# Optimization experiments

Hardware: AMD Instinct MI355X
Metric: run time of the kernel (lower is better)

Reference implementation:

```python
import jax, jax.numpy as jnp
import numpy as np

E = 65536          # number of edges (cell pairs)
D = 256            # hidden_dim
P = 8              # n_lr_pairs


def setup_inputs() -> dict:
    key = jax.random.key(0)
    k1, k2, k3, k4, k5, k6, k7 = jax.random.split(key, 7)
    scale = 1.0 / np.sqrt(D)
    z_src = jax.random.normal(k1, (E, D), dtype=jnp.float32)
    z_dst = jax.random.normal(k2, (E, D), dtype=jnp.float32)
    lr_pair_idx = jax.random.randint(k3, (E,), 0, P, dtype=jnp.int64)
    # Per-LR-pair Linear(D, D): y = x @ W.T + b  (torch convention, W: [out, in])
    W_lr = jax.random.normal(k4, (P, D, D), dtype=jnp.float32) * scale
    b_lr = jax.random.normal(k5, (P, D), dtype=jnp.float32) * scale
    # nn.Bilinear(D, D, 1): weight [1, D, D], bias [1]
    W_bil = jax.random.normal(k6, (1, D, D), dtype=jnp.float32) * scale
    b_bil = jax.random.normal(k7, (1,), dtype=jnp.float32) * scale
    return {"z_src": z_src, "z_dst": z_dst, "W_lr": W_lr, "b_lr": b_lr,
            "W_bil": W_bil, "b_bil": b_bil, "lr_pair_idx": lr_pair_idx}


def _forward(z_src, z_dst, W_lr, b_lr, W_bil, b_bil, lr_pair_idx):
    # Per-LR-pair linear projection of z_src (MoE-style routing).
    # Fixed small loop over P experts; each iteration is a dense GEMM over
    # all E edges, masked to the edges routed to that pair. All idx values
    # lie in [0, P), so the zeros-init in the original is fully overwritten.
    z_proj = jnp.zeros_like(z_src)
    for p in range(P):
        mask = (lr_pair_idx == p)[:, None]                      # [E, 1]
        y_p = z_src @ W_lr[p].T + b_lr[p]                       # [E, D]
        z_proj = jnp.where(mask, y_p, z_proj)
    # Bilinear scoring: score_e = z_proj_e @ W_bil[0] @ z_dst_e + b_bil
    t = z_proj @ W_bil[0]                                       # [E, D]
    scores = jnp.sum(t * z_dst, axis=-1, keepdims=True) + b_bil  # [E, 1]
    return scores


def reference(z_src, z_dst, W_lr, b_lr, W_bil, b_bil, lr_pair_idx):
    return _forward(z_src, z_dst, W_lr, b_lr, W_bil, b_bil, lr_pair_idx)
```

## Files before the change

### kernel.cpp

```cpp
#include <hip/hip_runtime.h>
#include <hip/hip_bf16.h>
#include <cstddef>

#define NE 65536
#define ND 256
#define NP 8
#define RBLK 64
#define EPB (NE / RBLK)

typedef short bf16x8 __attribute__((ext_vector_type(8)));
typedef float f32x4  __attribute__((ext_vector_type(4)));

__device__ __forceinline__ unsigned short f2bf(float f) {
  unsigned int u = __float_as_uint(f);
  u += 0x7FFFu + ((u >> 16) & 1u);
  return (unsigned short)(u >> 16);
}

__device__ __forceinline__ int sniff_is32(const void* idxraw, int* lflag) {
  int tid = threadIdx.x;
  if (tid == 0) *lflag = 0;
  __syncthreads();
  const unsigned int* w = (const unsigned int*)idxraw;
  unsigned int val = w[(blockIdx.x * 256 + tid) * 2 + 1];
  if (__any(val != 0) && (tid & 63) == 0) atomicOr(lflag, 1);
  __syncthreads();
  return *lflag;
}

__device__ __forceinline__ int load_idx(const void* idxraw, int is32, int e) {
  return is32 ? ((const int*)idxraw)[e] : (int)((const long long*)idxraw)[e];
}

__global__ __launch_bounds__(256) void k_hist(const void* __restrict__ idxraw,
                                              int* __restrict__ counts) {
  __shared__ int h[NP];
  __shared__ int lflag;
  int tid = threadIdx.x;
  int is32 = sniff_is32(idxraw, &lflag);
  if (tid < NP) h[tid] = 0;
  __syncthreads();
  int base = blockIdx.x * EPB;
#pragma unroll
  for (int i = 0; i < EPB / 256; ++i) {
    int p = load_idx(idxraw, is32, base + tid + i * 256);
    atomicAdd(&h[p], 1);
  }
  __syncthreads();
  if (tid < NP) counts[blockIdx.x * NP + tid] = h[tid];
}

__global__ __launch_bounds__(64) void k_scan(const int* __restrict__ counts,
                                             int* __restrict__ hdr,
                                             int* __restrict__ bases) {
  __shared__ int cnt[NP];
  __shared__ int off[NP + 1];
  int q = threadIdx.x;
  if (q < NP) {
    int s = 0;
    for (int b = 0; b < RBLK; ++b) s += counts[b * NP + q];
    cnt[q] = s;
  }
  __syncthreads();
  if (q == 0) {
    int o = 0, tt = 0;
    for (int p = 0; p < NP; ++p) {
      off[p] = o;
      hdr[p] = o;
      hdr[9 + p] = tt;
      o += cnt[p];
      tt += (cnt[p] + 63) >> 6;
    }
    off[NP] = o;
    hdr[NP] = o;
    hdr[9 + NP] = tt;
  }
  __syncthreads();
  if (q < NP) {
    int run = off[q];
    for (int b = 0; b < RBLK; ++b) {
      bases[b * NP + q] = run;
      run += counts[b * NP + q];
    }
  }
}

__global__ __launch_bounds__(256) void k_scatter(const void* __restrict__ idxraw,
                                                 const int* __restrict__ bases,
                                                 int* __restrict__ perm) {
  __shared__ int cur[NP];
  __shared__ int lflag;
  int tid = threadIdx.x;
  int is32 = sniff_is32(idxraw, &lflag);
  if (tid < NP) cur[tid] = bases[blockIdx.x * NP + tid];
  __syncthreads();
  int base = blockIdx.x * EPB;
#pragma unroll
  for (int i = 0; i < EPB / 256; ++i) {
    int e = base + tid + i * 256;
    int p = load_idx(idxraw, is32, e);
    int slot = atomicAdd(&cur[p], 1);
    perm[slot] = e;
  }
}

__global__ __launch_bounds__(256) void k_prep(const float* __restrict__ Wbil,
                                              const float* __restrict__ blr,
                                              unsigned short* __restrict__ WbT,
                                              float* __restrict__ v) {
  int b = blockIdx.x, t = threadIdx.x;
  if (b < 32) {
    int s = b * 256 + t;
    int kt = s >> 10, c = (s >> 6) & 15, l = s & 63;
    int col = c * 16 + (l & 15);
    int k0 = kt * 32 + (l >> 4) * 8;
    union { uint4 u; unsigned short h[8]; } uu;
#pragma unroll
    for (int j = 0; j < 8; ++j)
      uu.h[j] = f2bf(Wbil[(k0 + j) * ND + col]);
    *(uint4*)(WbT + (size_t)s * 8) = uu.u;
  } else {
    int p = b - 32;
    float s = 0.f;
    for (int k = 0; k < ND; ++k)
      s = fmaf(blr[p * ND + k], Wbil[k * ND + t], s);
    v[p * ND + t] = s;
  }
}

__global__ __launch_bounds__(256) void k_cpre(const float* __restrict__ Wlr,
                                              const unsigned short* __restrict__ WbT,
                                              unsigned short* __restrict__ Cst) {
  __shared__ unsigned short aF[2048 * 8];
  int blk = blockIdx.x;
  int p = blk >> 2;
  int i0 = (blk & 3) * 64;
  int tid = threadIdx.x;
  const float* Wp = Wlr + (size_t)p * ND * ND;
#pragma unroll
  for (int it = 0; it < 8; ++it) {
    int s = tid + it * 256;
    int kt = s >> 8, r = (s >> 6) & 3, l = s & 63;
    int i = r * 16 + (l & 15);
    int k0 = kt * 32 + (l >> 4) * 8;
    union { uint4 u; unsigned short h[8]; } uu;
#pragma unroll
    for (int j = 0; j < 8; ++j)
      uu.h[j] = f2bf(Wp[(size_t)(k0 + j) * ND + i0 + i]);
    *(uint4*)(aF + (size_t)s * 8) = uu.u;
  }
  __syncthreads();
  int w = tid >> 6, l = tid & 63;
  f32x4 zero = {0.f, 0.f, 0.f, 0.f};
  f32x4 acc[16];
#pragma unroll
  for (int c = 0; c < 16; ++c) acc[c] = zero;
  for (int kt = 0; kt < 8; ++kt) {
    bf16x8 a = *(const bf16x8*)(aF + (size_t)((kt * 4 + w) * 64 + l) * 8);
#pragma unroll
    for (int c = 0; c < 16; ++c) {
      bf16x8 bb = *(const bf16x8*)(WbT + (size_t)((kt * 16 + c) * 64 + l) * 8);
      acc[c] = __builtin_amdgcn_mfma_f32_16x16x32_bf16(a, bb, acc[c], 0, 0, 0);
    }
  }
  unsigned short* Cp = Cst + (size_t)p * ND * ND;
#pragma unroll
  for (int c = 0; c < 16; ++c) {
#pragma unroll
    for (int q = 0; q < 4; ++q) {
      int i = i0 + w * 16 + ((l >> 4) * 4) + q;
      int j = c * 16 + (l & 15);
      int pos = ((i >> 5) * 16 + (j >> 4)) * 512 + (((i >> 3) & 3) * 16 + (j & 15)) * 8 + (i & 7);
      Cp[pos] = f2bf(acc[c][q]);
    }
  }
}

__global__ __launch_bounds__(256, 2) void k_main(const float* __restrict__ zsrc,
                                                 const float* __restrict__ zdst,
                                                 const int* __restrict__ perm,
                                                 const int* __restrict__ hdr,
                                                 const unsigned short* __restrict__ Cst,
                                                 const float* __restrict__ v,
                                                 const float* __restrict__ bbil,
                                                 float* __restrict__ out) {
  __shared__ unsigned short aF[2048 * 8];
  __shared__ unsigned short zL[64 * 256];
  __shared__ int eids[64];
  __shared__ int shdr[18];
  __shared__ float red[4][64];
  int tid = threadIdx.x;
  if (tid < 18) shdr[tid] = hdr[tid];
  __syncthreads();
  int bid = blockIdx.x;
  if (bid >= shdr[9 + NP]) return;
  int p = 0;
  while (p < NP - 1 && bid >= shdr[9 + p + 1]) ++p;
  int t = bid - shdr[9 + p];
  int cnt = shdr[p + 1] - shdr[p];
  int ebase = shdr[p] + t * 64;
  int nrow = cnt - t * 64; if (nrow > 64) nrow = 64;
  if (tid < 64) {
    int r = tid < nrow ? tid : nrow - 1;
    eids[tid] = perm[ebase + r];
  }
  __syncthreads();
  int w = tid >> 6, l = tid & 63;
#pragma unroll
  for (int i = 0; i < 16; ++i) {
    int row = w * 16 + i;
    int e = eids[row];
    f32x4 fs = ((const f32x4*)(zsrc + (size_t)e * ND))[l];
    f32x4 fd = ((const f32x4*)(zdst + (size_t)e * ND))[l];
    union { ushort4 u; unsigned short h[4]; } us, ud;
#pragma unroll
    for (int j = 0; j < 4; ++j) { us.h[j] = f2bf(fs[j]); ud.h[j] = f2bf(fd[j]); }
    *(ushort4*)((char*)zL + row * 512 + l * 8) = ud.u;
    int slot = ((l >> 3) * 4 + w) * 64 + ((l & 7) >> 1) * 16 + i;
    *(ushort4*)((char*)aF + slot * 16 + (l & 1) * 8) = us.u;
  }
  __syncthreads();

  const unsigned short* Cp = Cst + (size_t)p * ND * ND;
  f32x4 zero = {0.f, 0.f, 0.f, 0.f};
  f32x4 acc[4][4];
#pragma unroll
  for (int r = 0; r < 4; ++r)
#pragma unroll
    for (int c = 0; c < 4; ++c) acc[r][c] = zero;
#pragma unroll
  for (int kt = 0; kt < 8; ++kt) {
    bf16x8 a[4];
#pragma unroll
    for (int r = 0; r < 4; ++r)
      a[r] = *(const bf16x8*)(aF + (size_t)((kt * 4 + r) * 64 + l) * 8);
#pragma unroll
    for (int cl = 0; cl < 4; ++cl) {
      bf16x8 bb = *(const bf16x8*)(Cp + (size_t)((kt * 16 + w * 4 + cl) * 64 + l) * 8);
#pragma unroll
      for (int r = 0; r < 4; ++r)
        acc[r][cl] = __builtin_amdgcn_mfma_f32_16x16x32_bf16(a[r], bb, acc[r][cl], 0, 0, 0);
    }
  }
  float vloc[4];
#pragma unroll
  for (int cl = 0; cl < 4; ++cl)
    vloc[cl] = v[p * ND + (w * 4 + cl) * 16 + (l & 15)];
#pragma unroll
  for (int r = 0; r < 4; ++r) {
#pragma unroll
    for (int q = 0; q < 4; ++q) {
      int row = r * 16 + ((l >> 4) * 4) + q;
      float sv = 0.f;
#pragma unroll
      for (int cl = 0; cl < 4; ++cl) {
        int col = (w * 4 + cl) * 16 + (l & 15);
        unsigned short hz = zL[row * 256 + col];
        float zv = __uint_as_float(((unsigned int)hz) << 16);
        sv = fmaf(acc[r][cl][q] + vloc[cl], zv, sv);
      }
      sv += __shfl_xor(sv, 1, 64);
      sv += __shfl_xor(sv, 2, 64);
      sv += __shfl_xor(sv, 4, 64);
      sv += __shfl_xor(sv, 8, 64);
      if ((l & 15) == 0) red[w][row] = sv;
    }
  }
  __syncthreads();
  if (tid < 64 && tid < nrow) {
    float sc = red[0][tid] + red[1][tid] + red[2][tid] + red[3][tid] + bbil[0];
    out[eids[tid]] = sc;
  }
}

extern "C" void kernel_launch(void* const* d_in, const int* in_sizes, int n_in,
                              void* d_out, int out_size, void* d_ws, size_t ws_size,
                              hipStream_t stream) {
  const float* zsrc = (const float*)d_in[0];
  const float* zdst = (const float*)d_in[1];
  const float* Wlr  = (const float*)d_in[2];
  const float* blr  = (const float*)d_in[3];
  const float* Wbil = (const float*)d_in[4];
  const float* bbil = (const float*)d_in[5];
  const void*  idx  = (const void*)d_in[6];
  float* out = (float*)d_out;

  char* ws = (char*)d_ws;
  int* hdr    = (int*)ws;
  int* counts = (int*)(ws + 4096);
  int* bases  = (int*)(ws + 8192);
  int* perm   = (int*)(ws + 16384);
  unsigned short* WbT = (unsigned short*)(ws + 16384 + (size_t)NE * 4);
  float* v = (float*)(ws + 16384 + (size_t)NE * 4 + 131072);
  unsigned short* Cst = (unsigned short*)(ws + 16384 + (size_t)NE * 4 + 131072 + 8192);

  k_prep<<<40, 256, 0, stream>>>(Wbil, blr, WbT, v);
  k_hist<<<RBLK, 256, 0, stream>>>(idx, counts);
  k_scan<<<1, 64, 0, stream>>>(counts, hdr, bases);
  k_scatter<<<RBLK, 256, 0, stream>>>(idx, bases, perm);
  k_cpre<<<32, 256, 0, stream>>>(Wlr, WbT, Cst);
  k_main<<<1032, 256, 0, stream>>>(zsrc, zdst, perm, hdr, Cst, v, bbil, out);
}
```

Baseline: 88.96 us.

## Pre-permute bf16 activations into tile-packed buffers during scatter, contiguous loads in main

Adds a scatter kernel that, besides building the permutation, gathers z_src and z_dst rows, converts them to bf16, and writes them into per-tile packed buffers already laid out as MFMA fragments and swizzled LDS rows. The main kernel then streams each 32KB tile contiguously into LDS instead of gathering fp32 rows per edge. The histogram and scatter grids grow to 256 blocks, and the zdst LDS layout gets an XOR swizzle to reduce bank conflicts. The cost is an extra write and read of packed bf16 activations through global memory, plus an extra kernel stage. A fallback path keeps the old gather when the workspace is too small.

```diff
diff --git a/kernel.cpp b/kernel.cpp
--- a/kernel.cpp
+++ b/kernel.cpp
@@ -1,12 +1,14 @@
 #include <hip/hip_runtime.h>
 #include <hip/hip_bf16.h>
 #include <cstddef>
+#include <cstdint>
 
 #define NE 65536
 #define ND 256
 #define NP 8
-#define RBLK 64
+#define RBLK 256
 #define EPB (NE / RBLK)
+#define MAXT 1032
 
 typedef short bf16x8 __attribute__((ext_vector_type(8)));
 typedef float f32x4  __attribute__((ext_vector_type(4)));
@@ -22,7 +24,7 @@
   if (tid == 0) *lflag = 0;
   __syncthreads();
   const unsigned int* w = (const unsigned int*)idxraw;
-  unsigned int val = w[(blockIdx.x * 256 + tid) * 2 + 1];
+  unsigned int val = w[((blockIdx.x & 63) * 256 + tid) * 2 + 1];
   if (__any(val != 0) && (tid & 63) == 0) atomicOr(lflag, 1);
   __syncthreads();
   return *lflag;
@@ -40,12 +42,8 @@
   int is32 = sniff_is32(idxraw, &lflag);
   if (tid < NP) h[tid] = 0;
   __syncthreads();
-  int base = blockIdx.x * EPB;
-#pragma unroll
-  for (int i = 0; i < EPB / 256; ++i) {
-    int p = load_idx(idxraw, is32, base + tid + i * 256);
-    atomicAdd(&h[p], 1);
-  }
+  int p = load_idx(idxraw, is32, blockIdx.x * EPB + tid);
+  atomicAdd(&h[p], 1);
   __syncthreads();
   if (tid < NP) counts[blockIdx.x * NP + tid] = h[tid];
 }
@@ -65,15 +63,11 @@
   if (q == 0) {
     int o = 0, tt = 0;
     for (int p = 0; p < NP; ++p) {
-      off[p] = o;
-      hdr[p] = o;
-      hdr[9 + p] = tt;
+      off[p] = o; hdr[p] = o; hdr[9 + p] = tt;
       o += cnt[p];
       tt += (cnt[p] + 63) >> 6;
     }
-    off[NP] = o;
-    hdr[NP] = o;
-    hdr[9 + NP] = tt;
+    off[NP] = o; hdr[NP] = o; hdr[9 + NP] = tt;
   }
   __syncthreads();
   if (q < NP) {
@@ -85,6 +79,50 @@
   }
 }
 
+__global__ __launch_bounds__(256) void k_scatter_mv(const void* __restrict__ idxraw,
+                                                    const float* __restrict__ zsrc,
+                                                    const float* __restrict__ zdst,
+                                                    const int* __restrict__ hdr,
+                                                    const int* __restrict__ bases,
+                                                    int* __restrict__ perm,
+                                                    unsigned short* __restrict__ zsrcP,
+                                                    unsigned short* __restrict__ zdstP) {
+  __shared__ int cur[NP];
+  __shared__ int soff[NP], stb[NP];
+  __shared__ int lflag;
+  int tid = threadIdx.x;
+  int is32 = sniff_is32(idxraw, &lflag);
+  if (tid < NP) {
+    cur[tid] = bases[blockIdx.x * NP + tid];
+    soff[tid] = hdr[tid];
+    stb[tid] = hdr[9 + tid];
+  }
+  __syncthreads();
+  int w = tid >> 6, l = tid & 63;
+  int e = blockIdx.x * EPB + w * 64 + l;
+  int p = load_idx(idxraw, is32, e);
+  int slot = atomicAdd(&cur[p], 1);
+  perm[slot] = e;
+  int local = slot - soff[p];
+  int tile = stb[p] + (local >> 6);
+  int row = local & 63;
+  int c0 = l * 4;
+#pragma unroll 8
+  for (int i = 0; i < 64; ++i) {
+    int ei = __shfl(e, i, 64);
+    int ti = __shfl(tile, i, 64);
+    int ri = __shfl(row, i, 64);
+    float4 fs = *(const float4*)(zsrc + (size_t)ei * ND + c0);
+    float4 fd = *(const float4*)(zdst + (size_t)ei * ND + c0);
+    union { unsigned long long u; unsigned short h[4]; } us, ud;
+    us.h[0] = f2bf(fs.x); us.h[1] = f2bf(fs.y); us.h[2] = f2bf(fs.z); us.h[3] = f2bf(fs.w);
+    ud.h[0] = f2bf(fd.x); ud.h[1] = f2bf(fd.y); ud.h[2] = f2bf(fd.z); ud.h[3] = f2bf(fd.w);
+    int fslot = ((c0 >> 5) * 4 + (ri >> 4)) * 64 + ((c0 & 31) >> 3) * 16 + (ri & 15);
+    *(unsigned long long*)((char*)zsrcP + (size_t)ti * 32768 + fslot * 16 + (c0 & 7) * 2) = us.u;
+    *(unsigned long long*)((char*)zdstP + (size_t)ti * 32768 + ri * 512 + ((l * 8) ^ ((ri & 7) << 4))) = ud.u;
+  }
+}
+
 __global__ __launch_bounds__(256) void k_scatter(const void* __restrict__ idxraw,
                                                  const int* __restrict__ bases,
                                                  int* __restrict__ perm) {
@@ -94,14 +132,10 @@
   int is32 = sniff_is32(idxraw, &lflag);
   if (tid < NP) cur[tid] = bases[blockIdx.x * NP + tid];
   __syncthreads();
-  int base = blockIdx.x * EPB;
-#pragma unroll
-  for (int i = 0; i < EPB / 256; ++i) {
-    int e = base + tid + i * 256;
-    int p = load_idx(idxraw, is32, e);
-    int slot = atomicAdd(&cur[p], 1);
-    perm[slot] = e;
-  }
+  int e = blockIdx.x * EPB + tid;
+  int p = load_idx(idxraw, is32, e);
+  int slot = atomicAdd(&cur[p], 1);
+  perm[slot] = e;
 }
 
 __global__ __launch_bounds__(256) void k_prep(const float* __restrict__ Wbil,
@@ -176,14 +210,14 @@
   }
 }
 
-__global__ __launch_bounds__(256, 2) void k_main(const float* __restrict__ zsrc,
-                                                 const float* __restrict__ zdst,
-                                                 const int* __restrict__ perm,
-                                                 const int* __restrict__ hdr,
-                                                 const unsigned short* __restrict__ Cst,
-                                                 const float* __restrict__ v,
-                                                 const float* __restrict__ bbil,
-                                                 float* __restrict__ out) {
+__global__ __launch_bounds__(256, 2) void k_main_f(const unsigned short* __restrict__ zsrcP,
+                                                   const unsigned short* __restrict__ zdstP,
+                                                   const int* __restrict__ perm,
+                                                   const int* __restrict__ hdr,
+                                                   const unsigned short* __restrict__ Cst,
+                                                   const float* __restrict__ v,
+                                                   const float* __restrict__ bbil,
+                                                   float* __restrict__ out) {
   __shared__ unsigned short aF[2048 * 8];
   __shared__ unsigned short zL[64 * 256];
   __shared__ int eids[64];
@@ -200,10 +234,100 @@
   int cnt = shdr[p + 1] - shdr[p];
   int ebase = shdr[p] + t * 64;
   int nrow = cnt - t * 64; if (nrow > 64) nrow = 64;
-  if (tid < 64) {
-    int r = tid < nrow ? tid : nrow - 1;
-    eids[tid] = perm[ebase + r];
-  }
+  if (tid < 64) eids[tid] = perm[ebase + (tid < nrow ? tid : nrow - 1)];
+  const uint4* gA = (const uint4*)((const char*)zsrcP + (size_t)bid * 32768);
+  const uint4* gZ = (const uint4*)((const char*)zdstP + (size_t)bid * 32768);
+  uint4 ra[8], rz[8];
+#pragma unroll
+  for (int i = 0; i < 8; ++i) ra[i] = gA[i * 256 + tid];
+#pragma unroll
+  for (int i = 0; i < 8; ++i) rz[i] = gZ[i * 256 + tid];
+#pragma unroll
+  for (int i = 0; i < 8; ++i) ((uint4*)aF)[i * 256 + tid] = ra[i];
+#pragma unroll
+  for (int i = 0; i < 8; ++i) ((uint4*)zL)[i * 256 + tid] = rz[i];
+  __syncthreads();
+
+  int w = tid >> 6, l = tid & 63;
+  const unsigned short* Cp = Cst + (size_t)p * ND * ND;
+  f32x4 zero = {0.f, 0.f, 0.f, 0.f};
+  f32x4 acc[4][4];
+#pragma unroll
+  for (int r = 0; r < 4; ++r)
+#pragma unroll
+    for (int c = 0; c < 4; ++c) acc[r][c] = zero;
+#pragma unroll
+  for (int kt = 0; kt < 8; ++kt) {
+    bf16x8 a[4];
+#pragma unroll
+    for (int r = 0; r < 4; ++r)
+      a[r] = *(const bf16x8*)(aF + (size_t)((kt * 4 + r) * 64 + l) * 8);
+#pragma unroll
+    for (int cl = 0; cl < 4; ++cl) {
+      bf16x8 bb = *(const bf16x8*)(Cp + (size_t)((kt * 16 + w * 4 + cl) * 64 + l) * 8);
+#pragma unroll
+      for (int r = 0; r < 4; ++r)
+        acc[r][cl] = __builtin_amdgcn_mfma_f32_16x16x32_bf16(a[r], bb, acc[r][cl], 0, 0, 0);
+    }
+  }
+  float vloc[4];
+#pragma unroll
+  for (int cl = 0; cl < 4; ++cl)
+    vloc[cl] = v[p * ND + (w * 4 + cl) * 16 + (l & 15)];
+#pragma unroll
+  for (int r = 0; r < 4; ++r) {
+#pragma unroll
+    for (int q = 0; q < 4; ++q) {
+      int row = r * 16 + ((l >> 4) * 4) + q;
+      unsigned int swz = (unsigned int)((row & 7) << 4);
+      float sv = 0.f;
+#pragma unroll
+      for (int cl = 0; cl < 4; ++cl) {
+        int col = (w * 4 + cl) * 16 + (l & 15);
+        unsigned int zb = (unsigned int)(row * 512) + (((unsigned int)(col * 2)) ^ swz);
+        unsigned short hz = *(const unsigned short*)((const char*)zL + zb);
+        float zv = __uint_as_float(((unsigned int)hz) << 16);
+        sv = fmaf(acc[r][cl][q] + vloc[cl], zv, sv);
+      }
+      sv += __shfl_xor(sv, 1, 64);
+      sv += __shfl_xor(sv, 2, 64);
+      sv += __shfl_xor(sv, 4, 64);
+      sv += __shfl_xor(sv, 8, 64);
+      if ((l & 15) == 0) red[w][row] = sv;
+    }
+  }
+  __syncthreads();
+  if (tid < 64 && tid < nrow) {
+    float sc = red[0][tid] + red[1][tid] + red[2][tid] + red[3][tid] + bbil[0];
+    out[eids[tid]] = sc;
+  }
+}
+
+__global__ __launch_bounds__(256, 2) void k_main_g(const float* __restrict__ zsrc,
+                                                   const float* __restrict__ zdst,
+                                                   const int* __restrict__ perm,
+                                                   const int* __restrict__ hdr,
+                                                   const unsigned short* __restrict__ Cst,
+                                                   const float* __restrict__ v,
+                                                   const float* __restrict__ bbil,
+                                                   float* __restrict__ out) {
+  __shared__ unsigned short aF[2048 * 8];
+  __shared__ unsigned short zL[64 * 256];
+  __shared__ int eids[64];
+  __shared__ int shdr[18];
+  __shared__ float red[4][64];
+  int tid = threadIdx.x;
+  if (tid < 18) shdr[tid] = hdr[tid];
+  __syncthreads();
+  int bid = blockIdx.x;
+  if (bid >= shdr[9 + NP]) return;
+  int p = 0;
+  while (p < NP - 1 && bid >= shdr[9 + p + 1]) ++p;
+  int t = bid - shdr[9 + p];
+  int cnt = shdr[p + 1] - shdr[p];
+  int ebase = shdr[p] + t * 64;
+  int nrow = cnt - t * 64; if (nrow > 64) nrow = 64;
+  if (tid < 64) eids[tid] = perm[ebase + (tid < nrow ? tid : nrow - 1)];
   __syncthreads();
   int w = tid >> 6, l = tid & 63;
 #pragma unroll
@@ -215,12 +339,11 @@
     union { ushort4 u; unsigned short h[4]; } us, ud;
 #pragma unroll
     for (int j = 0; j < 4; ++j) { us.h[j] = f2bf(fs[j]); ud.h[j] = f2bf(fd[j]); }
-    *(ushort4*)((char*)zL + row * 512 + l * 8) = ud.u;
+    *(ushort4*)((char*)zL + row * 512 + ((l * 8) ^ ((row & 7) << 4))) = ud.u;
     int slot = ((l >> 3) * 4 + w) * 64 + ((l & 7) >> 1) * 16 + i;
     *(ushort4*)((char*)aF + slot * 16 + (l & 1) * 8) = us.u;
   }
   __syncthreads();
-
   const unsigned short* Cp = Cst + (size_t)p * ND * ND;
   f32x4 zero = {0.f, 0.f, 0.f, 0.f};
   f32x4 acc[4][4];
@@ -251,11 +374,13 @@
 #pragma unroll
     for (int q = 0; q < 4; ++q) {
       int row = r * 16 + ((l >> 4) * 4) + q;
+      unsigned int swz = (unsigned int)((row & 7) << 4);
       float sv = 0.f;
 #pragma unroll
       for (int cl = 0; cl < 4; ++cl) {
         int col = (w * 4 + cl) * 16 + (l & 15);
-        unsigned short hz = zL[row * 256 + col];
+        unsigned int zb = (unsigned int)(row * 512) + (((unsigned int)(col * 2)) ^ swz);
+        unsigned short hz = *(const unsigned short*)((const char*)zL + zb);
         float zv = __uint_as_float(((unsigned int)hz) << 16);
         sv = fmaf(acc[r][cl][q] + vloc[cl], zv, sv);
       }
@@ -288,16 +413,25 @@
   char* ws = (char*)d_ws;
   int* hdr    = (int*)ws;
   int* counts = (int*)(ws + 4096);
-  int* bases  = (int*)(ws + 8192);
-  int* perm   = (int*)(ws + 16384);
-  unsigned short* WbT = (unsigned short*)(ws + 16384 + (size_t)NE * 4);
-  float* v = (float*)(ws + 16384 + (size_t)NE * 4 + 131072);
-  unsigned short* Cst = (unsigned short*)(ws + 16384 + (size_t)NE * 4 + 131072 + 8192);
+  int* bases  = (int*)(ws + 12288);
+  int* perm   = (int*)(ws + 20480);
+  unsigned short* WbT = (unsigned short*)(ws + 282624);
+  float* v            = (float*)(ws + 413696);
+  unsigned short* Cst = (unsigned short*)(ws + 421888);
+  size_t zoff = 2097152;
+  unsigned short* zsrcP = (unsigned short*)(ws + zoff);
+  unsigned short* zdstP = (unsigned short*)(ws + zoff + (size_t)MAXT * 32768);
+  size_t need = zoff + 2ull * (size_t)MAXT * 32768;
 
   k_prep<<<40, 256, 0, stream>>>(Wbil, blr, WbT, v);
   k_hist<<<RBLK, 256, 0, stream>>>(idx, counts);
   k_scan<<<1, 64, 0, stream>>>(counts, hdr, bases);
-  k_scatter<<<RBLK, 256, 0, stream>>>(idx, bases, perm);
   k_cpre<<<32, 256, 0, stream>>>(Wlr, WbT, Cst);
-  k_main<<<1032, 256, 0, stream>>>(zsrc, zdst, perm, hdr, Cst, v, bbil, out);
-}
+  if (ws_size >= need) {
+    k_scatter_mv<<<RBLK, 256, 0, stream>>>(idx, zsrc, zdst, hdr, bases, perm, zsrcP, zdstP);
+    k_main_f<<<MAXT, 256, 0, stream>>>(zsrcP, zdstP, perm, hdr, Cst, v, bbil, out);
+  } else {
+    k_scatter<<<RBLK, 256, 0, stream>>>(idx, bases, perm);
+    k_main_g<<<MAXT, 256, 0, stream>>>(zsrc, zdst, perm, hdr, Cst, v, bbil, out);
+  }
+}
```

New measurement: 128.9 us. +44.9%, slower.

## Use 512-thread blocks in main kernel with XOR-swizzled LDS layouts

Applied to the files above, without the earlier changes.

The main fused kernel goes from 256 to 512 threads per block, so each of 8 waves handles half as many output column tiles and the accumulator register footprint halves. Launch bounds now ask for 4 blocks per CU. LDS writes and reads for the staged z_src fragments and z_dst rows get XOR swizzles to cut bank conflicts, and the final reduction sums 8 partial buffers. The risk is more B-operand (Cst) loads per block and higher LDS use per CU, which may cap how many blocks actually fit.

```diff
diff --git a/kernel.cpp b/kernel.cpp
--- a/kernel.cpp
+++ b/kernel.cpp
@@ -7,6 +7,7 @@
 #define NP 8
 #define RBLK 64
 #define EPB (NE / RBLK)
+#define MAXT 1032
 
 typedef short bf16x8 __attribute__((ext_vector_type(8)));
 typedef float f32x4  __attribute__((ext_vector_type(4)));
@@ -16,18 +17,20 @@
   u += 0x7FFFu + ((u >> 16) & 1u);
   return (unsigned short)(u >> 16);
 }
+__device__ __forceinline__ float bf2f(unsigned short h) {
+  return __uint_as_float(((unsigned int)h) << 16);
+}
 
 __device__ __forceinline__ int sniff_is32(const void* idxraw, int* lflag) {
   int tid = threadIdx.x;
   if (tid == 0) *lflag = 0;
   __syncthreads();
   const unsigned int* w = (const unsigned int*)idxraw;
-  unsigned int val = w[(blockIdx.x * 256 + tid) * 2 + 1];
+  unsigned int val = w[((blockIdx.x & 63) * 256 + (tid & 255)) * 2 + 1];
   if (__any(val != 0) && (tid & 63) == 0) atomicOr(lflag, 1);
   __syncthreads();
   return *lflag;
 }
-
 __device__ __forceinline__ int load_idx(const void* idxraw, int is32, int e) {
   return is32 ? ((const int*)idxraw)[e] : (int)((const long long*)idxraw)[e];
 }
@@ -65,15 +68,11 @@
   if (q == 0) {
     int o = 0, tt = 0;
     for (int p = 0; p < NP; ++p) {
-      off[p] = o;
-      hdr[p] = o;
-      hdr[9 + p] = tt;
+      off[p] = o; hdr[p] = o; hdr[9 + p] = tt;
       o += cnt[p];
       tt += (cnt[p] + 63) >> 6;
     }
-    off[NP] = o;
-    hdr[NP] = o;
-    hdr[9 + NP] = tt;
+    off[NP] = o; hdr[NP] = o; hdr[9 + NP] = tt;
   }
   __syncthreads();
   if (q < NP) {
@@ -176,7 +175,7 @@
   }
 }
 
-__global__ __launch_bounds__(256, 2) void k_main(const float* __restrict__ zsrc,
+__global__ __launch_bounds__(512, 4) void k_main(const float* __restrict__ zsrc,
                                                  const float* __restrict__ zdst,
                                                  const int* __restrict__ perm,
                                                  const int* __restrict__ hdr,
@@ -184,11 +183,11 @@
                                                  const float* __restrict__ v,
                                                  const float* __restrict__ bbil,
                                                  float* __restrict__ out) {
-  __shared__ unsigned short aF[2048 * 8];
-  __shared__ unsigned short zL[64 * 256];
+  __shared__ unsigned short aF[16384];
+  __shared__ unsigned short zL[16384];
+  __shared__ float red[8][64];
   __shared__ int eids[64];
   __shared__ int shdr[18];
-  __shared__ float red[4][64];
   int tid = threadIdx.x;
   if (tid < 18) shdr[tid] = hdr[tid];
   __syncthreads();
@@ -200,64 +199,69 @@
   int cnt = shdr[p + 1] - shdr[p];
   int ebase = shdr[p] + t * 64;
   int nrow = cnt - t * 64; if (nrow > 64) nrow = 64;
-  if (tid < 64) {
-    int r = tid < nrow ? tid : nrow - 1;
-    eids[tid] = perm[ebase + r];
-  }
+  if (tid < 64) eids[tid] = perm[ebase + (tid < nrow ? tid : nrow - 1)];
   __syncthreads();
   int w = tid >> 6, l = tid & 63;
-#pragma unroll
-  for (int i = 0; i < 16; ++i) {
-    int row = w * 16 + i;
+
+  int kt0 = l >> 3, pos0 = (l & 7) >> 1, par0 = l & 1;
+#pragma unroll
+  for (int i = 0; i < 8; ++i) {
+    int row = w * 8 + i;
     int e = eids[row];
-    f32x4 fs = ((const f32x4*)(zsrc + (size_t)e * ND))[l];
-    f32x4 fd = ((const f32x4*)(zdst + (size_t)e * ND))[l];
-    union { ushort4 u; unsigned short h[4]; } us, ud;
-#pragma unroll
-    for (int j = 0; j < 4; ++j) { us.h[j] = f2bf(fs[j]); ud.h[j] = f2bf(fd[j]); }
-    *(ushort4*)((char*)zL + row * 512 + l * 8) = ud.u;
-    int slot = ((l >> 3) * 4 + w) * 64 + ((l & 7) >> 1) * 16 + i;
-    *(ushort4*)((char*)aF + slot * 16 + (l & 1) * 8) = us.u;
+    float4 fs = *(const float4*)(zsrc + (size_t)e * ND + l * 4);
+    float4 fd = *(const float4*)(zdst + (size_t)e * ND + l * 4);
+    union { ushort4 u; unsigned short hh[4]; } us, ud;
+    us.hh[0] = f2bf(fs.x); us.hh[1] = f2bf(fs.y); us.hh[2] = f2bf(fs.z); us.hh[3] = f2bf(fs.w);
+    ud.hh[0] = f2bf(fd.x); ud.hh[1] = f2bf(fd.y); ud.hh[2] = f2bf(fd.z); ud.hh[3] = f2bf(fd.w);
+    *(ushort4*)((char*)zL + row * 512 + ((l * 8) ^ ((row & 7) << 4))) = ud.u;
+    unsigned byte = (unsigned)(((kt0 * 4 + (row >> 4)) << 10) | (pos0 << 8) | ((row & 15) << 4) | (par0 << 3));
+    byte ^= (unsigned)(((kt0 & 3) << 5) ^ ((pos0 & 1) << 4));
+    *(ushort4*)((char*)aF + byte) = us.u;
   }
   __syncthreads();
 
   const unsigned short* Cp = Cst + (size_t)p * ND * ND;
   f32x4 zero = {0.f, 0.f, 0.f, 0.f};
-  f32x4 acc[4][4];
-#pragma unroll
-  for (int r = 0; r < 4; ++r)
-#pragma unroll
-    for (int c = 0; c < 4; ++c) acc[r][c] = zero;
+  f32x4 acc[4][2];
+#pragma unroll
+  for (int sr = 0; sr < 4; ++sr)
+#pragma unroll
+    for (int cl = 0; cl < 2; ++cl) acc[sr][cl] = zero;
+  int pos = l >> 4;
 #pragma unroll
   for (int kt = 0; kt < 8; ++kt) {
     bf16x8 a[4];
 #pragma unroll
-    for (int r = 0; r < 4; ++r)
-      a[r] = *(const bf16x8*)(aF + (size_t)((kt * 4 + r) * 64 + l) * 8);
-#pragma unroll
-    for (int cl = 0; cl < 4; ++cl) {
-      bf16x8 bb = *(const bf16x8*)(Cp + (size_t)((kt * 16 + w * 4 + cl) * 64 + l) * 8);
-#pragma unroll
-      for (int r = 0; r < 4; ++r)
-        acc[r][cl] = __builtin_amdgcn_mfma_f32_16x16x32_bf16(a[r], bb, acc[r][cl], 0, 0, 0);
-    }
-  }
-  float vloc[4];
-#pragma unroll
-  for (int cl = 0; cl < 4; ++cl)
-    vloc[cl] = v[p * ND + (w * 4 + cl) * 16 + (l & 15)];
-#pragma unroll
-  for (int r = 0; r < 4; ++r) {
+    for (int sr = 0; sr < 4; ++sr) {
+      unsigned byte = (unsigned)(((kt * 4 + sr) << 10) | (pos << 8) | ((l & 15) << 4));
+      byte ^= (unsigned)(((kt & 3) << 5) ^ ((pos & 1) << 4));
+      a[sr] = *(const bf16x8*)((const char*)aF + byte);
+    }
+#pragma unroll
+    for (int cl = 0; cl < 2; ++cl) {
+      bf16x8 bb = *(const bf16x8*)(Cp + (size_t)((kt * 16 + (w * 2 + cl)) * 64 + l) * 8);
+#pragma unroll
+      for (int sr = 0; sr < 4; ++sr)
+        acc[sr][cl] = __builtin_amdgcn_mfma_f32_16x16x32_bf16(a[sr], bb, acc[sr][cl], 0, 0, 0);
+    }
+  }
+
+  float vloc[2];
+#pragma unroll
+  for (int cl = 0; cl < 2; ++cl)
+    vloc[cl] = v[p * ND + (w * 2 + cl) * 16 + (l & 15)];
+#pragma unroll
+  for (int sr = 0; sr < 4; ++sr) {
 #pragma unroll
     for (int q = 0; q < 4; ++q) {
-      int row = r * 16 + ((l >> 4) * 4) + q;
+      int row = sr * 16 + (l >> 4) * 4 + q;
+      unsigned swz = (unsigned)((row & 7) << 4);
       float sv = 0.f;
 #pragma unroll
-      for (int cl = 0; cl < 4; ++cl) {
-        int col = (w * 4 + cl) * 16 + (l & 15);
-        unsigned short hz = zL[row * 256 + col];
-        float zv = __uint_as_float(((unsigned int)hz) << 16);
-        sv = fmaf(acc[r][cl][q] + vloc[cl], zv, sv);
+      for (int cl = 0; cl < 2; ++cl) {
+        int col = (w * 2 + cl) * 16 + (l & 15);
+        unsigned zb = (unsigned)(row * 512) + (((unsigned)(col * 2)) ^ swz);
+        sv = fmaf(acc[sr][cl][q] + vloc[cl], bf2f(*(const unsigned short*)((const char*)zL + zb)), sv);
       }
       sv += __shfl_xor(sv, 1, 64);
       sv += __shfl_xor(sv, 2, 64);
@@ -268,7 +272,9 @@
   }
   __syncthreads();
   if (tid < 64 && tid < nrow) {
-    float sc = red[0][tid] + red[1][tid] + red[2][tid] + red[3][tid] + bbil[0];
+    float sc = bbil[0];
+#pragma unroll
+    for (int ww = 0; ww < 8; ++ww) sc += red[ww][tid];
     out[eids[tid]] = sc;
   }
 }
@@ -299,5 +305,5 @@
   k_scan<<<1, 64, 0, stream>>>(counts, hdr, bases);
   k_scatter<<<RBLK, 256, 0, stream>>>(idx, bases, perm);
   k_cpre<<<32, 256, 0, stream>>>(Wlr, WbT, Cst);
-  k_main<<<1032, 256, 0, stream>>>(zsrc, zdst, perm, hdr, Cst, v, bbil, out);
-}
+  k_main<<<MAXT, 512, 0, stream>>>(zsrc, zdst, perm, hdr, Cst, v, bbil, out);
+}
```

Result: faster. 84.50 us (-5.0%).
